# Kernel tuning notes

Measured on AMD Instinct MI355X. Metric: run time of the kernel, lower is better.

The kernel has to match this reference:

```python
import math
import jax, jax.numpy as jnp
import numpy as np

Q = 0.15
B, T, D = 32, 2048, 512
NEG = -1e9


def setup_inputs() -> dict:
    key = jax.random.key(0)
    k1, k2 = jax.random.split(key)
    H = jax.random.normal(k1, (B, T, D), dtype=jnp.float32)
    lengths = jax.random.randint(k2, (B,), 1, T + 1, dtype=jnp.int32)
    return {"H": H, "lengths": lengths}


def reference(H, lengths):
    Bc, Tc, Dc = H.shape
    kmax = int(math.ceil(Tc * Q))  # static upper bound on per-row k

    # per-timestep L2 norm, masked beyond each row's length
    valid = jnp.arange(Tc)[None, :] < lengths[:, None]            # [B,T]
    scores = jnp.where(valid, jnp.linalg.norm(H, axis=2), NEG)    # [B,T]

    # per-row k = clamp(ceil(len*q), 1)
    k_vals = jnp.maximum(
        jnp.ceil(lengths.astype(jnp.float32) * Q).astype(jnp.int32), 1
    )                                                              # [B]

    # take a static top-kmax, then mask down to each row's dynamic k
    _, top_idx = jax.lax.top_k(scores, kmax)                      # [B,kmax]
    gathered = jnp.take_along_axis(H, top_idx[:, :, None], axis=1)  # [B,kmax,D]
    sel = (jnp.arange(kmax)[None, :] < k_vals[:, None]).astype(H.dtype)  # [B,kmax]

    pooled = jnp.einsum("bkd,bk->bd", gathered, sel) / k_vals[:, None].astype(H.dtype)
    return pooled
```

## Files before the change

kernel.cpp:

```cpp
#include <hip/hip_runtime.h>
#include <stdint.h>

static constexpr int BB = 32;
static constexpr int TT = 2048;
static constexpr int DD = 512;
static constexpr int LMAX = 320;

__global__ __launch_bounds__(256) void topq_norms(
    const float* __restrict__ H, const int* __restrict__ lengths,
    unsigned int* __restrict__ keys)
{
    const int wave = threadIdx.x >> 6;
    const int lane = threadIdx.x & 63;
    const int row  = (blockIdx.x << 2) + wave;
    const float4* p = reinterpret_cast<const float4*>(H) + (size_t)row * (DD / 4);
    float4 a = p[lane];
    float4 c = p[lane + 64];
    float s = a.x*a.x + a.y*a.y + a.z*a.z + a.w*a.w
            + c.x*c.x + c.y*c.y + c.z*c.z + c.w*c.w;
    #pragma unroll
    for (int off = 32; off; off >>= 1) s += __shfl_xor(s, off);
    if (lane == 0) {
        const int b = row >> 11;
        const int t = row & (TT - 1);
        unsigned int key = 0u;
        if (t < lengths[b]) key = __float_as_uint(sqrtf(s)) + 1u;
        keys[row] = key;
    }
}

__global__ __launch_bounds__(512) void topq_selpool(
    const unsigned int* __restrict__ keys, const int* __restrict__ lengths,
    const float* __restrict__ H, float* __restrict__ out)
{
    __shared__ unsigned int   sk[TT];
    __shared__ unsigned short slist[LMAX];
    __shared__ int scount;
    __shared__ int skk;

    const int b   = blockIdx.x;
    const int tid = threadIdx.x;
    for (int i = tid; i < TT; i += 512) sk[i] = keys[b * TT + i];
    if (tid == 0) scount = 0;
    __syncthreads();

    if (tid < 64) {
        const int lane = tid;
        unsigned int kreg[32];
        #pragma unroll
        for (int j = 0; j < 32; ++j) kreg[j] = sk[j * 64 + lane];

        const int len = lengths[b];
        int k = (int)ceilf((float)len * 0.15f);
        if (k < 1) k = 1;

        unsigned long long lo = 0, hi = 1ull << 43;
        while (hi - lo > 1ull) {
            const unsigned long long mid = (lo + hi) >> 1;
            int cnt = 0;
            #pragma unroll
            for (int j = 0; j < 32; ++j) {
                const unsigned long long ck =
                    ((unsigned long long)kreg[j] << 11) |
                    (unsigned long long)(TT - 1 - (j * 64 + lane));
                cnt += (ck >= mid) ? 1 : 0;
            }
            #pragma unroll
            for (int off = 32; off; off >>= 1) cnt += __shfl_xor(cnt, off);
            if (cnt >= k) lo = mid; else hi = mid;
        }
        #pragma unroll
        for (int j = 0; j < 32; ++j) {
            const unsigned long long ck =
                ((unsigned long long)kreg[j] << 11) |
                (unsigned long long)(TT - 1 - (j * 64 + lane));
            if (ck >= lo) {
                const int p = atomicAdd(&scount, 1);
                slist[p] = (unsigned short)(j * 64 + lane);
            }
        }
        if (tid == 0) skk = k;
    }
    __syncthreads();

    const int k = skk;
    const float* Hb = H + (size_t)b * TT * DD;
    float a0 = 0.f, a1 = 0.f, a2 = 0.f, a3 = 0.f,
          a4 = 0.f, a5 = 0.f, a6 = 0.f, a7 = 0.f;
    int j = 0;
    for (; j + 8 <= k; j += 8) {
        const int t0 = slist[j],     t1 = slist[j + 1],
                  t2 = slist[j + 2], t3 = slist[j + 3],
                  t4 = slist[j + 4], t5 = slist[j + 5],
                  t6 = slist[j + 6], t7 = slist[j + 7];
        a0 += Hb[(size_t)t0 * DD + tid];
        a1 += Hb[(size_t)t1 * DD + tid];
        a2 += Hb[(size_t)t2 * DD + tid];
        a3 += Hb[(size_t)t3 * DD + tid];
        a4 += Hb[(size_t)t4 * DD + tid];
        a5 += Hb[(size_t)t5 * DD + tid];
        a6 += Hb[(size_t)t6 * DD + tid];
        a7 += Hb[(size_t)t7 * DD + tid];
    }
    for (; j < k; ++j) a0 += Hb[(size_t)slist[j] * DD + tid];
    const float s = ((a0 + a1) + (a2 + a3)) + ((a4 + a5) + (a6 + a7));
    out[b * DD + tid] = s / (float)k;
}

extern "C" void kernel_launch(void* const* d_in, const int* in_sizes, int n_in,
                              void* d_out, int out_size, void* d_ws, size_t ws_size,
                              hipStream_t stream)
{
    const float* H       = (const float*)d_in[0];
    const int*   lengths = (const int*)d_in[1];
    float*       out     = (float*)d_out;

    unsigned int* keys = (unsigned int*)d_ws;

    topq_norms  <<<dim3(BB * TT / 4), 256, 0, stream>>>(H, lengths, keys);
    topq_selpool<<<dim3(BB),          512, 0, stream>>>(keys, lengths, H, out);
}
```

Before: 215.6 us.

## Split pooling across column blocks, narrow selection search, batch rows per wave

The norm kernel now has each wave handle four rows, interleaving the shuffle reductions and storing keys as one uint4. The selection kernel bounds its binary search by the min/max key and searches 32-bit values instead of 43-bit composites. It then resolves ties by index order with a ballot scan. Pooling is split over a 4-way grid in y with float4 loads and a shared-memory reduction across 16 row groups, raising block count from 32 to 128. Each of the four column blocks repeats the whole top-k selection, which adds redundant work.

```diff
diff --git a/kernel.cpp b/kernel.cpp
--- a/kernel.cpp
+++ b/kernel.cpp
@@ -12,20 +12,32 @@
 {
     const int wave = threadIdx.x >> 6;
     const int lane = threadIdx.x & 63;
-    const int row  = (blockIdx.x << 2) + wave;
-    const float4* p = reinterpret_cast<const float4*>(H) + (size_t)row * (DD / 4);
-    float4 a = p[lane];
-    float4 c = p[lane + 64];
-    float s = a.x*a.x + a.y*a.y + a.z*a.z + a.w*a.w
-            + c.x*c.x + c.y*c.y + c.z*c.z + c.w*c.w;
+    const int base = (blockIdx.x * 4 + wave) * 4;
+    const int b    = base >> 11;
+    const int len  = lengths[b];
+    const float4* p = reinterpret_cast<const float4*>(H) + (size_t)base * (DD / 4);
+
+    float s[4];
     #pragma unroll
-    for (int off = 32; off; off >>= 1) s += __shfl_xor(s, off);
+    for (int r = 0; r < 4; ++r) {
+        float4 a = p[r * (DD / 4) + lane];
+        float4 c = p[r * (DD / 4) + lane + 64];
+        s[r] = a.x*a.x + a.y*a.y + a.z*a.z + a.w*a.w
+             + c.x*c.x + c.y*c.y + c.z*c.z + c.w*c.w;
+    }
+    #pragma unroll
+    for (int off = 32; off; off >>= 1) {
+        #pragma unroll
+        for (int r = 0; r < 4; ++r) s[r] += __shfl_xor(s[r], off);
+    }
     if (lane == 0) {
-        const int b = row >> 11;
-        const int t = row & (TT - 1);
-        unsigned int key = 0u;
-        if (t < lengths[b]) key = __float_as_uint(sqrtf(s)) + 1u;
-        keys[row] = key;
+        const int t0 = base & (TT - 1);
+        uint4 kv;
+        kv.x = (t0 + 0 < len) ? __float_as_uint(sqrtf(s[0])) + 1u : 0u;
+        kv.y = (t0 + 1 < len) ? __float_as_uint(sqrtf(s[1])) + 1u : 0u;
+        kv.z = (t0 + 2 < len) ? __float_as_uint(sqrtf(s[2])) + 1u : 0u;
+        kv.w = (t0 + 3 < len) ? __float_as_uint(sqrtf(s[3])) + 1u : 0u;
+        *reinterpret_cast<uint4*>(keys + base) = kv;
     }
 }
 
@@ -35,12 +47,16 @@
 {
     __shared__ unsigned int   sk[TT];
     __shared__ unsigned short slist[LMAX];
+    __shared__ float4 sred[16][32];
     __shared__ int scount;
     __shared__ int skk;
 
     const int b   = blockIdx.x;
+    const int q   = blockIdx.y;
     const int tid = threadIdx.x;
-    for (int i = tid; i < TT; i += 512) sk[i] = keys[b * TT + i];
+
+    reinterpret_cast<uint4*>(sk)[tid] =
+        reinterpret_cast<const uint4*>(keys + b * TT)[tid];
     if (tid == 0) scount = 0;
     __syncthreads();
 
@@ -54,57 +70,116 @@
         int k = (int)ceilf((float)len * 0.15f);
         if (k < 1) k = 1;
 
-        unsigned long long lo = 0, hi = 1ull << 43;
-        while (hi - lo > 1ull) {
-            const unsigned long long mid = (lo + hi) >> 1;
+        unsigned int mn = 0xFFFFFFFFu, mx = 0u;
+        #pragma unroll
+        for (int j = 0; j < 32; ++j) {
+            const unsigned int kk = kreg[j];
+            if (kk != 0u && kk < mn) mn = kk;
+            if (kk > mx) mx = kk;
+        }
+        #pragma unroll
+        for (int off = 32; off; off >>= 1) {
+            const unsigned int mno = (unsigned int)__shfl_xor((int)mn, off);
+            const unsigned int mxo = (unsigned int)__shfl_xor((int)mx, off);
+            mn = mn < mno ? mn : mno;
+            mx = mx > mxo ? mx : mxo;
+        }
+
+        unsigned int lo = mn, hi = mx + 1u;
+        while (hi - lo > 1u) {
+            const unsigned int mid = lo + ((hi - lo) >> 1);
             int cnt = 0;
             #pragma unroll
-            for (int j = 0; j < 32; ++j) {
-                const unsigned long long ck =
-                    ((unsigned long long)kreg[j] << 11) |
-                    (unsigned long long)(TT - 1 - (j * 64 + lane));
-                cnt += (ck >= mid) ? 1 : 0;
-            }
+            for (int j = 0; j < 32; ++j) cnt += (kreg[j] >= mid) ? 1 : 0;
             #pragma unroll
             for (int off = 32; off; off >>= 1) cnt += __shfl_xor(cnt, off);
             if (cnt >= k) lo = mid; else hi = mid;
         }
+        const unsigned int v = lo;
+
+        int cgt = 0, ceq = 0;
         #pragma unroll
         for (int j = 0; j < 32; ++j) {
-            const unsigned long long ck =
-                ((unsigned long long)kreg[j] << 11) |
-                (unsigned long long)(TT - 1 - (j * 64 + lane));
-            if (ck >= lo) {
+            cgt += (kreg[j] > v)  ? 1 : 0;
+            ceq += (kreg[j] == v) ? 1 : 0;
+        }
+        #pragma unroll
+        for (int off = 32; off; off >>= 1) {
+            cgt += __shfl_xor(cgt, off);
+            ceq += __shfl_xor(ceq, off);
+        }
+        const int m = k - cgt;
+
+        #pragma unroll
+        for (int j = 0; j < 32; ++j) {
+            if (kreg[j] > v) {
                 const int p = atomicAdd(&scount, 1);
                 slist[p] = (unsigned short)(j * 64 + lane);
             }
         }
-        if (tid == 0) skk = k;
+        if (m == ceq) {
+            #pragma unroll
+            for (int j = 0; j < 32; ++j) {
+                if (kreg[j] == v) {
+                    const int p = atomicAdd(&scount, 1);
+                    slist[p] = (unsigned short)(j * 64 + lane);
+                }
+            }
+        } else {
+            const unsigned long long ltmask = (1ull << lane) - 1ull;
+            int taken = 0;
+            for (int c = 0; c < TT / 64 && taken < m; ++c) {
+                const int t = c * 64 + lane;
+                const bool pred = (sk[t] == v);
+                const unsigned long long mask = __ballot(pred);
+                const int rank = taken + __popcll(mask & ltmask);
+                if (pred && rank < m) {
+                    const int p = atomicAdd(&scount, 1);
+                    slist[p] = (unsigned short)t;
+                }
+                taken += __popcll(mask);
+            }
+        }
+        if (lane == 0) skk = k;
     }
     __syncthreads();
 
-    const int k = skk;
-    const float* Hb = H + (size_t)b * TT * DD;
-    float a0 = 0.f, a1 = 0.f, a2 = 0.f, a3 = 0.f,
-          a4 = 0.f, a5 = 0.f, a6 = 0.f, a7 = 0.f;
-    int j = 0;
-    for (; j + 8 <= k; j += 8) {
-        const int t0 = slist[j],     t1 = slist[j + 1],
-                  t2 = slist[j + 2], t3 = slist[j + 3],
-                  t4 = slist[j + 4], t5 = slist[j + 5],
-                  t6 = slist[j + 6], t7 = slist[j + 7];
-        a0 += Hb[(size_t)t0 * DD + tid];
-        a1 += Hb[(size_t)t1 * DD + tid];
-        a2 += Hb[(size_t)t2 * DD + tid];
-        a3 += Hb[(size_t)t3 * DD + tid];
-        a4 += Hb[(size_t)t4 * DD + tid];
-        a5 += Hb[(size_t)t5 * DD + tid];
-        a6 += Hb[(size_t)t6 * DD + tid];
-        a7 += Hb[(size_t)t7 * DD + tid];
+    const int k  = skk;
+    const int r  = tid >> 5;
+    const int cg = tid & 31;
+    const float4* Hb4 =
+        reinterpret_cast<const float4*>(H + (size_t)b * TT * DD);
+    const int col4 = q * 32 + cg;
+
+    float4 a0 = {0.f, 0.f, 0.f, 0.f}, a1 = {0.f, 0.f, 0.f, 0.f};
+    int j = r;
+    for (; j + 16 < k; j += 32) {
+        const int t0 = slist[j], t1 = slist[j + 16];
+        const float4 x0 = Hb4[(size_t)t0 * 128 + col4];
+        const float4 x1 = Hb4[(size_t)t1 * 128 + col4];
+        a0.x += x0.x; a0.y += x0.y; a0.z += x0.z; a0.w += x0.w;
+        a1.x += x1.x; a1.y += x1.y; a1.z += x1.z; a1.w += x1.w;
     }
-    for (; j < k; ++j) a0 += Hb[(size_t)slist[j] * DD + tid];
-    const float s = ((a0 + a1) + (a2 + a3)) + ((a4 + a5) + (a6 + a7));
-    out[b * DD + tid] = s / (float)k;
+    if (j < k) {
+        const float4 x0 = Hb4[(size_t)slist[j] * 128 + col4];
+        a0.x += x0.x; a0.y += x0.y; a0.z += x0.z; a0.w += x0.w;
+    }
+    a0.x += a1.x; a0.y += a1.y; a0.z += a1.z; a0.w += a1.w;
+    sred[r][cg] = a0;
+    __syncthreads();
+
+    if (tid < 32) {
+        float4 s = {0.f, 0.f, 0.f, 0.f};
+        #pragma unroll
+        for (int rr = 0; rr < 16; ++rr) {
+            const float4 x = sred[rr][tid];
+            s.x += x.x; s.y += x.y; s.z += x.z; s.w += x.w;
+        }
+        const float kf = (float)k;
+        float4 o;
+        o.x = s.x / kf; o.y = s.y / kf; o.z = s.z / kf; o.w = s.w / kf;
+        reinterpret_cast<float4*>(out)[b * 128 + q * 32 + tid] = o;
+    }
 }
 
 extern "C" void kernel_launch(void* const* d_in, const int* in_sizes, int n_in,
@@ -117,6 +192,6 @@
 
     unsigned int* keys = (unsigned int*)d_ws;
 
-    topq_norms  <<<dim3(BB * TT / 4), 256, 0, stream>>>(H, lengths, keys);
-    topq_selpool<<<dim3(BB),          512, 0, stream>>>(keys, lengths, H, out);
+    topq_norms  <<<dim3(BB * TT / 16), 256, 0, stream>>>(H, lengths, keys);
+    topq_selpool<<<dim3(BB, 4),        512, 0, stream>>>(keys, lengths, H, out);
 }
```

After: 204.3 us, median of 2. 5.2% less time.
